# Kernel tuning notes

Hardware: AMD Instinct MI355X
Metric: run time of the kernel (lower is better)

Reference implementation:

```python
import jax, jax.numpy as jnp
import numpy as np

N_NODES = 100000
N_EDGES = 1600000
NUM_FEATURES = 128
HIDDEN = 64
NUM_CLASSES = 16


def setup_inputs() -> dict:
    key = jax.random.key(0)
    k1, k2, k3, k4 = jax.random.split(key, 4)
    x = jax.random.normal(k1, (N_NODES, NUM_FEATURES), dtype=jnp.float32)
    edge_index = jax.random.randint(k2, (2, N_EDGES), 0, N_NODES, dtype=jnp.int64)
    # Glorot-ish scaled weights ([in, out] layout; PyG stores [out,in] but math is x @ W)
    W1 = jax.random.normal(k3, (NUM_FEATURES, HIDDEN), dtype=jnp.float32) * (1.0 / np.sqrt(NUM_FEATURES))
    W2 = jax.random.normal(k4, (HIDDEN, NUM_CLASSES), dtype=jnp.float32) * (1.0 / np.sqrt(HIDDEN))
    return {"x": x, "edge_index": edge_index, "W1": W1, "W2": W2}


def _gcn_conv(x, edge_index, W):
    # GCNConv(add_self_loops=False, bias=False): linear then sym-normalized scatter-add.
    n = x.shape[0]
    row, col = edge_index[0], edge_index[1]  # source -> target
    h = x @ W  # [N, out]
    # degree from unit edge weights scattered on target nodes
    deg = jax.ops.segment_sum(jnp.ones(row.shape[0], dtype=h.dtype), col, num_segments=n)
    deg_inv_sqrt = jnp.where(deg > 0, jax.lax.rsqrt(jnp.maximum(deg, 1.0)), 0.0)
    norm = deg_inv_sqrt[row] * deg_inv_sqrt[col]  # [E]
    msg = h[row] * norm[:, None]  # gather + scale, [E, out]
    return jax.ops.segment_sum(msg, col, num_segments=n)  # scatter-add to targets


def reference(x, edge_index, W1, W2):
    h = _gcn_conv(x, edge_index, W1)
    h = _gcn_conv(h, edge_index, W2)
    return jax.nn.log_softmax(h, axis=1)
```

## Files before the change

kernel.cpp:

```cpp
#include <hip/hip_runtime.h>
#include <hip/hip_bf16.h>
#include <hip/hip_fp16.h>


#define STRIDE 48
#define BCAP   3072
#define SRTCAP 6272


__global__ __launch_bounds__(1024) void k_bucket(const int* __restrict__ ei,
                                                 const void* __restrict__ xv,
                                                 const void* __restrict__ W1v,
                                                 const void* __restrict__ W2v,
                                                 int* __restrict__ flags,
                                                 float* __restrict__ W12,
                                                 int* __restrict__ bcnt,
                                                 int* __restrict__ buf,
                                                 int e, int n, int nb, int epb) {
    __shared__ int hist[1024];
    __shared__ int scn[1024];
    __shared__ int cur[1024];
    __shared__ int gb[1024];
    __shared__ float wtmp[2048];
    __shared__ int srt[SRTCAP];
    __shared__ unsigned short key[SRTCAP];
    __shared__ int sraw, sbad, tot;
    int t = threadIdx.x;
    int b = blockIdx.x;

    if (t == 0) { sraw = 0; sbad = 0; }
    hist[t] = 0;
    __syncthreads();

    long long base_e = (long long)b * epb;
    int myE = e - (int)base_e;
    if (myE > epb) myE = epb;

    if (t < myE) {
        long long i = base_e + t;
        if (ei[2 * (size_t)i + 1] != 0) atomicOr(&sraw, 1);
    }
    if (b < 8) {
        const unsigned short* xs = (const unsigned short*)xv;
        if (t < 1024) {
            unsigned ex2 = (xs[t] >> 7) & 0xFF;
            if (ex2 >= 0x90) atomicOr(&sbad, 1);
        }
    }
    __syncthreads();
    int raw = sraw ? 0 : 1;

    if (b < 8) {
        bool f32 = sbad != 0;
        if (f32) {
            const float* W1 = (const float*)W1v;
            const float* W2 = (const float*)W2v;
            wtmp[t] = W1[b * 1024 + t];
            wtmp[1024 + t] = W2[t];
        } else {
            const __hip_bfloat16* W1 = (const __hip_bfloat16*)W1v;
            const __hip_bfloat16* W2 = (const __hip_bfloat16*)W2v;
            wtmp[t] = __bfloat162float(W1[b * 1024 + t]);
            wtmp[1024 + t] = __bfloat162float(W2[t]);
        }
    }

    int bk[7], rec[7];
#pragma unroll
    for (int j = 0; j < 7; ++j) {
        int li = j * 1024 + t;
        bk[j] = -1;
        if (li < myE) {
            long long i = base_e + li;
            int r, c;
            if (raw) {
                r = ((const int2*)ei)[(size_t)i].x;
                c = ((const int2*)ei)[(size_t)e + i].x;
            } else {
                r = ei[i];
                c = ei[(size_t)e + i];
            }
            if ((unsigned)c < (unsigned)n && (unsigned)r < (unsigned)n) {
                bk[j] = c >> 7;
                rec[j] = ((c & 127) << 17) | r;
                atomicAdd(&hist[bk[j]], 1);
            }
        }
    }
    __syncthreads();

    scn[t] = hist[t];
    __syncthreads();
#pragma unroll
    for (int off = 1; off < 1024; off <<= 1) {
        int add = (t >= off) ? scn[t - off] : 0;
        __syncthreads();
        scn[t] += add;
        __syncthreads();
    }
    {
        int h = hist[t];
        cur[t] = scn[t] - h;
        gb[t] = h ? atomicAdd(&bcnt[t], h) : 0;
        if (t == 1023) tot = scn[1023];
    }
    __syncthreads();

#pragma unroll
    for (int j = 0; j < 7; ++j) {
        if (bk[j] >= 0) {
            int s = atomicAdd(&cur[bk[j]], 1);
            srt[s] = rec[j];
            key[s] = (unsigned short)bk[j];
        }
    }
    __syncthreads();

    int total = tot;
    for (int i = t; i < total; i += 1024) {
        int k = key[i];
        int excl = cur[k] - hist[k];
        int slot = gb[k] + (i - excl);
        if (slot < BCAP) buf[(size_t)k * BCAP + slot] = srt[i];
    }

    if (b < 8 && t < 256) {
        int kl = t >> 4, c = t & 15;
        float acc = 0.0f;
#pragma unroll 8
        for (int f = 0; f < 64; ++f) acc += wtmp[kl * 64 + f] * wtmp[1024 + f * 16 + c];
        W12[(16 * b + kl) * 16 + c] = acc;
        if (b == 0 && t == 0) { flags[0] = sbad; flags[1] = raw; }
    }
}


__global__ __launch_bounds__(256) void k_csr_z(const int* __restrict__ bcnt,
                                               const int* __restrict__ buf,
                                               const void* __restrict__ xv,
                                               const float* __restrict__ W12,
                                               const int* __restrict__ flags,
                                               int* __restrict__ cnt,
                                               int* __restrict__ csr,
                                               __half* __restrict__ z, int n) {
    __shared__ int lcnt[128];
    __shared__ int lcsr[128 * STRIDE];
    __shared__ float ws[2048];
    int t = threadIdx.x;
    int b = blockIdx.x;
    if (t < 128) lcnt[t] = 0;
    int4 zero4 = {0, 0, 0, 0};
    for (int i = t; i < 128 * STRIDE / 4; i += 256) ((int4*)lcsr)[i] = zero4;
    for (int i = t; i < 2048; i += 256) ws[i] = W12[i];
    __syncthreads();

    int m = bcnt[b];
    if (m > BCAP) m = BCAP;
    for (int i = t; i < m; i += 256) {
        int rec = buf[(size_t)b * BCAP + i];
        int cl = rec >> 17;
        int r = rec & 0x1FFFF;
        int slot = atomicAdd(&lcnt[cl], 1);
        if (slot < STRIDE) lcsr[cl * STRIDE + slot] = r;
    }
    __syncthreads();

    {
        int node = (b << 7) + t;
        if (t < 128 && node < n) cnt[node] = lcnt[t];
    }
    const int4* src = (const int4*)lcsr;
    int4* dst = (int4*)csr + (size_t)b * (128 * STRIDE / 4);
    for (int i = t; i < 128 * STRIDE / 4; i += 256) dst[i] = src[i];

    int node_l = t >> 1;
    int kh = t & 1;
    int node0 = (b << 7) + node_l;
    if (node0 >= n) return;
    int node = node0;

    float acc[16];
#pragma unroll
    for (int c = 0; c < 16; ++c) acc[c] = 0.0f;

    if (flags[0]) {
        const float4* x4 = (const float4*)xv + (size_t)node * 32 + kh * 16;
#pragma unroll
        for (int j = 0; j < 16; ++j) {
            float4 v = x4[j];
            float xk[4] = {v.x, v.y, v.z, v.w};
#pragma unroll
            for (int q = 0; q < 4; ++q) {
                const float* w = &ws[(kh * 64 + j * 4 + q) * 16];
                float xx = xk[q];
#pragma unroll
                for (int c = 0; c < 16; ++c) acc[c] += xx * w[c];
            }
        }
    } else {
        const uint4* x4 = (const uint4*)xv + (size_t)node * 16 + kh * 8;
#pragma unroll
        for (int j = 0; j < 8; ++j) {
            uint4 v = x4[j];
            float xk[8];
            xk[0] = __uint_as_float(v.x << 16);
            xk[1] = __uint_as_float(v.x & 0xffff0000u);
            xk[2] = __uint_as_float(v.y << 16);
            xk[3] = __uint_as_float(v.y & 0xffff0000u);
            xk[4] = __uint_as_float(v.z << 16);
            xk[5] = __uint_as_float(v.z & 0xffff0000u);
            xk[6] = __uint_as_float(v.w << 16);
            xk[7] = __uint_as_float(v.w & 0xffff0000u);
#pragma unroll
            for (int q = 0; q < 8; ++q) {
                const float* w = &ws[(kh * 64 + j * 8 + q) * 16];
                float xx = xk[q];
#pragma unroll
                for (int c = 0; c < 16; ++c) acc[c] += xx * w[c];
            }
        }
    }

#pragma unroll
    for (int c = 0; c < 16; ++c) acc[c] += __shfl_xor(acc[c], 1);

    int deg = lcnt[node_l];
    float di = (deg > 0) ? rsqrtf((float)deg) : 0.0f;
    int c0 = kh * 8;
    __half2 hh[4];
#pragma unroll
    for (int j = 0; j < 4; ++j)
        hh[j] = __halves2half2(__float2half(acc[c0 + 2 * j] * di),
                               __float2half(acc[c0 + 2 * j + 1] * di));
    uint4 u;
    u.x = *(unsigned*)&hh[0]; u.y = *(unsigned*)&hh[1];
    u.z = *(unsigned*)&hh[2]; u.w = *(unsigned*)&hh[3];
    ((uint4*)(z + (size_t)node * 16))[kh] = u;
}


__global__ __launch_bounds__(256) void k_agg1b(const int* __restrict__ cnt,
                                               const int* __restrict__ csr,
                                               const __half* __restrict__ z,
                                               __half* __restrict__ z2, int n) {
    int t = threadIdx.x;
    int wid = t >> 6, lane = t & 63;
    int half = lane >> 5, l5 = lane & 31;
    int node0 = blockIdx.x * 8 + wid * 2 + half;
    int node = node0 < n ? node0 : n - 1;
    int id  = csr[(size_t)node * STRIDE + l5];
    int id2 = csr[(size_t)node * STRIDE + 32 + (l5 & 15)];
    int deg = cnt[node];
    float di = (deg > 0) ? rsqrtf((float)deg) : 0.0f;
    int m = deg < STRIDE ? deg : STRIDE;
    int sub = l5 >> 3, f2 = l5 & 7;
    int base = half << 5;
    const __half2* zp = (const __half2*)z;
    float ax = 0.0f, ay = 0.0f;
#pragma unroll
    for (int j = 0; j < 24; j += 4) {
        int s = __shfl(id, base + j + sub);
        float2 v = __half22float2(zp[(size_t)s * 8 + f2]);
        bool ok = (j + sub) < m;
        ax += ok ? v.x : 0.0f;
        ay += ok ? v.y : 0.0f;
    }
    for (int j = 24; j < m; j += 4) {
        int sidx = j + sub;
        int s = (j < 32) ? __shfl(id, base + sidx)
                         : __shfl(id2, base + (sidx & 15));
        if (sidx < m) {
            float2 v = __half22float2(zp[(size_t)s * 8 + f2]);
            ax += v.x;
            ay += v.y;
        }
    }
    ax += __shfl_xor(ax, 8);  ay += __shfl_xor(ay, 8);
    ax += __shfl_xor(ax, 16); ay += __shfl_xor(ay, 16);
    float s2 = di * di;
    if (node0 < n && l5 < 8)
        ((__half2*)z2)[(size_t)node * 8 + l5] =
            __halves2half2(__float2half(ax * s2), __float2half(ay * s2));
}


__global__ __launch_bounds__(256) void k_agg2b(const int* __restrict__ cnt,
                                               const int* __restrict__ csr,
                                               const __half* __restrict__ z2,
                                               const int* __restrict__ flags,
                                               void* __restrict__ outv, int n) {
    int t = threadIdx.x;
    int wid = t >> 6, lane = t & 63;
    int half = lane >> 5, l5 = lane & 31;
    int node0 = blockIdx.x * 8 + wid * 2 + half;
    int node = node0 < n ? node0 : n - 1;
    int id  = csr[(size_t)node * STRIDE + l5];
    int id2 = csr[(size_t)node * STRIDE + 32 + (l5 & 15)];
    int deg = cnt[node];
    float di = (deg > 0) ? rsqrtf((float)deg) : 0.0f;
    int m = deg < STRIDE ? deg : STRIDE;
    int sub = l5 >> 3, f2 = l5 & 7;
    int base = half << 5;
    const __half2* zp = (const __half2*)z2;
    float ax = 0.0f, ay = 0.0f;
#pragma unroll
    for (int j = 0; j < 24; j += 4) {
        int s = __shfl(id, base + j + sub);
        float2 v = __half22float2(zp[(size_t)s * 8 + f2]);
        bool ok = (j + sub) < m;
        ax += ok ? v.x : 0.0f;
        ay += ok ? v.y : 0.0f;
    }
    for (int j = 24; j < m; j += 4) {
        int sidx = j + sub;
        int s = (j < 32) ? __shfl(id, base + sidx)
                         : __shfl(id2, base + (sidx & 15));
        if (sidx < m) {
            float2 v = __half22float2(zp[(size_t)s * 8 + f2]);
            ax += v.x;
            ay += v.y;
        }
    }
    ax += __shfl_xor(ax, 8);  ay += __shfl_xor(ay, 8);
    ax += __shfl_xor(ax, 16); ay += __shfl_xor(ay, 16);
    float vx = ax * di, vy = ay * di;
    float mx = fmaxf(vx, vy);
#pragma unroll
    for (int d = 1; d <= 4; d <<= 1) mx = fmaxf(mx, __shfl_xor(mx, d));
    float es = __expf(vx - mx) + __expf(vy - mx);
#pragma unroll
    for (int d = 1; d <= 4; d <<= 1) es += __shfl_xor(es, d);
    float ls = __logf(es);
    float rx = vx - mx - ls, ry = vy - mx - ls;
    if (node0 < n && l5 < 8) {
        if (flags[0]) {
            float2 r; r.x = rx; r.y = ry;
            ((float2*)outv)[(size_t)node * 8 + l5] = r;
        } else {
            __hip_bfloat162 hh;
            hh.x = __float2bfloat16(rx);
            hh.y = __float2bfloat16(ry);
            ((__hip_bfloat162*)outv)[(size_t)node * 8 + l5] = hh;
        }
    }
}


extern "C" void kernel_launch(void* const* d_in, const int* in_sizes, int n_in,
                              void* d_out, int out_size, void* d_ws, size_t ws_size,
                              hipStream_t stream) {
    const int F = 128, C = 16;
    int n = in_sizes[0] / F;
    int e = in_sizes[1] / 2;
    int nb = (n + 127) >> 7;

    const void* x = d_in[0];
    const int* ei = (const int*)d_in[1];
    const void* W1 = d_in[2];
    const void* W2 = d_in[3];

    char* p = (char*)d_ws;
    auto carve = [&](size_t bytes) {
        char* r = p;
        p += (bytes + 255) & ~(size_t)255;
        return r;
    };
    int*    flags = (int*)  carve(256);
    int*    bcnt  = (int*)  carve((size_t)nb * 4);
    int*    cnt   = (int*)  carve((size_t)n * 4);
    float*  W12   = (float*)carve(128 * 16 * 4);
    int*    csr   = (int*)  carve(((size_t)nb * 128 * STRIDE + 64) * 4);
    __half* z     = (__half*)carve((size_t)n * C * 2);
    size_t buf_sz = (size_t)nb * BCAP * 4;
    size_t z2_sz = (size_t)n * C * 2;
    char* regionB = carve(buf_sz > z2_sz ? buf_sz : z2_sz);
    int*    buf = (int*)regionB;
    __half* z2  = (__half*)regionB;
    (void)ws_size;

    int gb_bucket = (e + SRTCAP - 1) / SRTCAP;
    if (gb_bucket < 256) gb_bucket = 256;
    int epb = (e + gb_bucket - 1) / gb_bucket;

    hipMemsetAsync(bcnt, 0, (size_t)nb * 4, stream);
    k_bucket<<<gb_bucket, 1024, 0, stream>>>(ei, x, W1, W2, flags, W12, bcnt, buf, e, n, nb, epb);
    k_csr_z<<<nb, 256, 0, stream>>>(bcnt, buf, x, W12, flags, cnt, csr, z, n);
    k_agg1b<<<(n + 7) / 8, 256, 0, stream>>>(cnt, csr, z, z2, n);
    k_agg2b<<<(n + 7) / 8, 256, 0, stream>>>(cnt, csr, z2, flags, d_out, n);
}
```

Before: 159.8 us.

## Rebuild per-bucket CSR in shared memory inside each aggregation kernel

The first kernel no longer writes a global padded CSR and count array. It now only counts degrees. Each aggregation kernel instead rebuilds its bucket's adjacency lists in LDS from the bucket buffer and then processes 128 nodes per 512-thread block. This removes the global CSR write and the two strided CSR reads, and buf and z2 get separate workspace. In exchange the bucket-to-CSR scatter is done twice, each block uses a large LDS footprint, and the block count drops, which may cost occupancy and latency hiding.

```diff
diff --git a/kernel.cpp b/kernel.cpp
--- a/kernel.cpp
+++ b/kernel.cpp
@@ -42,10 +42,8 @@
     }
     if (b < 8) {
         const unsigned short* xs = (const unsigned short*)xv;
-        if (t < 1024) {
-            unsigned ex2 = (xs[t] >> 7) & 0xFF;
-            if (ex2 >= 0x90) atomicOr(&sbad, 1);
-        }
+        unsigned ex2 = (xs[t] >> 7) & 0xFF;
+        if (ex2 >= 0x90) atomicOr(&sbad, 1);
     }
     __syncthreads();
     int raw = sraw ? 0 : 1;
@@ -135,22 +133,17 @@
 }
 
 
-__global__ __launch_bounds__(256) void k_csr_z(const int* __restrict__ bcnt,
-                                               const int* __restrict__ buf,
-                                               const void* __restrict__ xv,
-                                               const float* __restrict__ W12,
-                                               const int* __restrict__ flags,
-                                               int* __restrict__ cnt,
-                                               int* __restrict__ csr,
-                                               __half* __restrict__ z, int n) {
+__global__ __launch_bounds__(256) void k_zd(const int* __restrict__ bcnt,
+                                            const int* __restrict__ buf,
+                                            const void* __restrict__ xv,
+                                            const float* __restrict__ W12,
+                                            const int* __restrict__ flags,
+                                            __half* __restrict__ z, int n) {
     __shared__ int lcnt[128];
-    __shared__ int lcsr[128 * STRIDE];
     __shared__ float ws[2048];
     int t = threadIdx.x;
     int b = blockIdx.x;
     if (t < 128) lcnt[t] = 0;
-    int4 zero4 = {0, 0, 0, 0};
-    for (int i = t; i < 128 * STRIDE / 4; i += 256) ((int4*)lcsr)[i] = zero4;
     for (int i = t; i < 2048; i += 256) ws[i] = W12[i];
     __syncthreads();
 
@@ -158,20 +151,9 @@
     if (m > BCAP) m = BCAP;
     for (int i = t; i < m; i += 256) {
         int rec = buf[(size_t)b * BCAP + i];
-        int cl = rec >> 17;
-        int r = rec & 0x1FFFF;
-        int slot = atomicAdd(&lcnt[cl], 1);
-        if (slot < STRIDE) lcsr[cl * STRIDE + slot] = r;
-    }
-    __syncthreads();
-
-    {
-        int node = (b << 7) + t;
-        if (t < 128 && node < n) cnt[node] = lcnt[t];
-    }
-    const int4* src = (const int4*)lcsr;
-    int4* dst = (int4*)csr + (size_t)b * (128 * STRIDE / 4);
-    for (int i = t; i < 128 * STRIDE / 4; i += 256) dst[i] = src[i];
+        atomicAdd(&lcnt[rec >> 17], 1);
+    }
+    __syncthreads();
 
     int node_l = t >> 1;
     int kh = t & 1;
@@ -239,108 +221,147 @@
 }
 
 
-__global__ __launch_bounds__(256) void k_agg1b(const int* __restrict__ cnt,
-                                               const int* __restrict__ csr,
+__global__ __launch_bounds__(512) void k_agg1n(const int* __restrict__ bcnt,
+                                               const int* __restrict__ buf,
                                                const __half* __restrict__ z,
                                                __half* __restrict__ z2, int n) {
+    __shared__ int lcnt[128];
+    __shared__ int lcsr[128 * STRIDE];
     int t = threadIdx.x;
+    int b = blockIdx.x;
+    if (t < 128) lcnt[t] = 0;
+    int4 zero4 = {0, 0, 0, 0};
+    for (int i = t; i < 128 * STRIDE / 4; i += 512) ((int4*)lcsr)[i] = zero4;
+    __syncthreads();
+
+    int m = bcnt[b];
+    if (m > BCAP) m = BCAP;
+    for (int i = t; i < m; i += 512) {
+        int rec = buf[(size_t)b * BCAP + i];
+        int cl = rec >> 17;
+        int r = rec & 0x1FFFF;
+        int slot = atomicAdd(&lcnt[cl], 1);
+        if (slot < STRIDE) lcsr[cl * STRIDE + slot] = r;
+    }
+    __syncthreads();
+
     int wid = t >> 6, lane = t & 63;
     int half = lane >> 5, l5 = lane & 31;
-    int node0 = blockIdx.x * 8 + wid * 2 + half;
-    int node = node0 < n ? node0 : n - 1;
-    int id  = csr[(size_t)node * STRIDE + l5];
-    int id2 = csr[(size_t)node * STRIDE + 32 + (l5 & 15)];
-    int deg = cnt[node];
-    float di = (deg > 0) ? rsqrtf((float)deg) : 0.0f;
-    int m = deg < STRIDE ? deg : STRIDE;
     int sub = l5 >> 3, f2 = l5 & 7;
-    int base = half << 5;
     const __half2* zp = (const __half2*)z;
-    float ax = 0.0f, ay = 0.0f;
-#pragma unroll
-    for (int j = 0; j < 24; j += 4) {
-        int s = __shfl(id, base + j + sub);
-        float2 v = __half22float2(zp[(size_t)s * 8 + f2]);
-        bool ok = (j + sub) < m;
-        ax += ok ? v.x : 0.0f;
-        ay += ok ? v.y : 0.0f;
-    }
-    for (int j = 24; j < m; j += 4) {
-        int sidx = j + sub;
-        int s = (j < 32) ? __shfl(id, base + sidx)
-                         : __shfl(id2, base + (sidx & 15));
-        if (sidx < m) {
+#pragma unroll
+    for (int it = 0; it < 8; ++it) {
+        int node_l = it * 16 + wid * 2 + half;
+        int node0 = (b << 7) + node_l;
+        int deg = lcnt[node_l];
+        float di = (deg > 0) ? rsqrtf((float)deg) : 0.0f;
+        int mm = deg < STRIDE ? deg : STRIDE;
+        int lb = node_l * STRIDE;
+        float ax = 0.0f, ay = 0.0f;
+#pragma unroll
+        for (int j = 0; j < 24; j += 4) {
+            int s = lcsr[lb + j + sub];
             float2 v = __half22float2(zp[(size_t)s * 8 + f2]);
-            ax += v.x;
-            ay += v.y;
-        }
-    }
-    ax += __shfl_xor(ax, 8);  ay += __shfl_xor(ay, 8);
-    ax += __shfl_xor(ax, 16); ay += __shfl_xor(ay, 16);
-    float s2 = di * di;
-    if (node0 < n && l5 < 8)
-        ((__half2*)z2)[(size_t)node * 8 + l5] =
-            __halves2half2(__float2half(ax * s2), __float2half(ay * s2));
+            bool ok = (j + sub) < mm;
+            ax += ok ? v.x : 0.0f;
+            ay += ok ? v.y : 0.0f;
+        }
+        for (int j = 24; j < mm; j += 4) {
+            int sidx = j + sub;
+            if (sidx < mm) {
+                int s = lcsr[lb + sidx];
+                float2 v = __half22float2(zp[(size_t)s * 8 + f2]);
+                ax += v.x;
+                ay += v.y;
+            }
+        }
+        ax += __shfl_xor(ax, 8);  ay += __shfl_xor(ay, 8);
+        ax += __shfl_xor(ax, 16); ay += __shfl_xor(ay, 16);
+        float s2 = di * di;
+        if (node0 < n && l5 < 8)
+            ((__half2*)z2)[(size_t)node0 * 8 + l5] =
+                __halves2half2(__float2half(ax * s2), __float2half(ay * s2));
+    }
 }
 
 
-__global__ __launch_bounds__(256) void k_agg2b(const int* __restrict__ cnt,
-                                               const int* __restrict__ csr,
+__global__ __launch_bounds__(512) void k_agg2n(const int* __restrict__ bcnt,
+                                               const int* __restrict__ buf,
                                                const __half* __restrict__ z2,
                                                const int* __restrict__ flags,
                                                void* __restrict__ outv, int n) {
+    __shared__ int lcnt[128];
+    __shared__ int lcsr[128 * STRIDE];
     int t = threadIdx.x;
+    int b = blockIdx.x;
+    if (t < 128) lcnt[t] = 0;
+    int4 zero4 = {0, 0, 0, 0};
+    for (int i = t; i < 128 * STRIDE / 4; i += 512) ((int4*)lcsr)[i] = zero4;
+    __syncthreads();
+
+    int m = bcnt[b];
+    if (m > BCAP) m = BCAP;
+    for (int i = t; i < m; i += 512) {
+        int rec = buf[(size_t)b * BCAP + i];
+        int cl = rec >> 17;
+        int r = rec & 0x1FFFF;
+        int slot = atomicAdd(&lcnt[cl], 1);
+        if (slot < STRIDE) lcsr[cl * STRIDE + slot] = r;
+    }
+    __syncthreads();
+
     int wid = t >> 6, lane = t & 63;
     int half = lane >> 5, l5 = lane & 31;
-    int node0 = blockIdx.x * 8 + wid * 2 + half;
-    int node = node0 < n ? node0 : n - 1;
-    int id  = csr[(size_t)node * STRIDE + l5];
-    int id2 = csr[(size_t)node * STRIDE + 32 + (l5 & 15)];
-    int deg = cnt[node];
-    float di = (deg > 0) ? rsqrtf((float)deg) : 0.0f;
-    int m = deg < STRIDE ? deg : STRIDE;
     int sub = l5 >> 3, f2 = l5 & 7;
-    int base = half << 5;
     const __half2* zp = (const __half2*)z2;
-    float ax = 0.0f, ay = 0.0f;
-#pragma unroll
-    for (int j = 0; j < 24; j += 4) {
-        int s = __shfl(id, base + j + sub);
-        float2 v = __half22float2(zp[(size_t)s * 8 + f2]);
-        bool ok = (j + sub) < m;
-        ax += ok ? v.x : 0.0f;
-        ay += ok ? v.y : 0.0f;
-    }
-    for (int j = 24; j < m; j += 4) {
-        int sidx = j + sub;
-        int s = (j < 32) ? __shfl(id, base + sidx)
-                         : __shfl(id2, base + (sidx & 15));
-        if (sidx < m) {
+    bool f32o = flags[0] != 0;
+#pragma unroll
+    for (int it = 0; it < 8; ++it) {
+        int node_l = it * 16 + wid * 2 + half;
+        int node0 = (b << 7) + node_l;
+        int deg = lcnt[node_l];
+        float di = (deg > 0) ? rsqrtf((float)deg) : 0.0f;
+        int mm = deg < STRIDE ? deg : STRIDE;
+        int lb = node_l * STRIDE;
+        float ax = 0.0f, ay = 0.0f;
+#pragma unroll
+        for (int j = 0; j < 24; j += 4) {
+            int s = lcsr[lb + j + sub];
             float2 v = __half22float2(zp[(size_t)s * 8 + f2]);
-            ax += v.x;
-            ay += v.y;
-        }
-    }
-    ax += __shfl_xor(ax, 8);  ay += __shfl_xor(ay, 8);
-    ax += __shfl_xor(ax, 16); ay += __shfl_xor(ay, 16);
-    float vx = ax * di, vy = ay * di;
-    float mx = fmaxf(vx, vy);
-#pragma unroll
-    for (int d = 1; d <= 4; d <<= 1) mx = fmaxf(mx, __shfl_xor(mx, d));
-    float es = __expf(vx - mx) + __expf(vy - mx);
-#pragma unroll
-    for (int d = 1; d <= 4; d <<= 1) es += __shfl_xor(es, d);
-    float ls = __logf(es);
-    float rx = vx - mx - ls, ry = vy - mx - ls;
-    if (node0 < n && l5 < 8) {
-        if (flags[0]) {
-            float2 r; r.x = rx; r.y = ry;
-            ((float2*)outv)[(size_t)node * 8 + l5] = r;
-        } else {
-            __hip_bfloat162 hh;
-            hh.x = __float2bfloat16(rx);
-            hh.y = __float2bfloat16(ry);
-            ((__hip_bfloat162*)outv)[(size_t)node * 8 + l5] = hh;
+            bool ok = (j + sub) < mm;
+            ax += ok ? v.x : 0.0f;
+            ay += ok ? v.y : 0.0f;
+        }
+        for (int j = 24; j < mm; j += 4) {
+            int sidx = j + sub;
+            if (sidx < mm) {
+                int s = lcsr[lb + sidx];
+                float2 v = __half22float2(zp[(size_t)s * 8 + f2]);
+                ax += v.x;
+                ay += v.y;
+            }
+        }
+        ax += __shfl_xor(ax, 8);  ay += __shfl_xor(ay, 8);
+        ax += __shfl_xor(ax, 16); ay += __shfl_xor(ay, 16);
+        float vx = ax * di, vy = ay * di;
+        float mx = fmaxf(vx, vy);
+#pragma unroll
+        for (int d = 1; d <= 4; d <<= 1) mx = fmaxf(mx, __shfl_xor(mx, d));
+        float es = __expf(vx - mx) + __expf(vy - mx);
+#pragma unroll
+        for (int d = 1; d <= 4; d <<= 1) es += __shfl_xor(es, d);
+        float ls = __logf(es);
+        float rx = vx - mx - ls, ry = vy - mx - ls;
+        if (node0 < n && l5 < 8) {
+            if (f32o) {
+                float2 r; r.x = rx; r.y = ry;
+                ((float2*)outv)[(size_t)node0 * 8 + l5] = r;
+            } else {
+                __hip_bfloat162 hh;
+                hh.x = __float2bfloat16(rx);
+                hh.y = __float2bfloat16(ry);
+                ((__hip_bfloat162*)outv)[(size_t)node0 * 8 + l5] = hh;
+            }
         }
     }
 }
@@ -367,15 +388,10 @@
     };
     int*    flags = (int*)  carve(256);
     int*    bcnt  = (int*)  carve((size_t)nb * 4);
-    int*    cnt   = (int*)  carve((size_t)n * 4);
     float*  W12   = (float*)carve(128 * 16 * 4);
-    int*    csr   = (int*)  carve(((size_t)nb * 128 * STRIDE + 64) * 4);
+    int*    buf   = (int*)  carve((size_t)nb * BCAP * 4);
     __half* z     = (__half*)carve((size_t)n * C * 2);
-    size_t buf_sz = (size_t)nb * BCAP * 4;
-    size_t z2_sz = (size_t)n * C * 2;
-    char* regionB = carve(buf_sz > z2_sz ? buf_sz : z2_sz);
-    int*    buf = (int*)regionB;
-    __half* z2  = (__half*)regionB;
+    __half* z2    = (__half*)carve((size_t)n * C * 2);
     (void)ws_size;
 
     int gb_bucket = (e + SRTCAP - 1) / SRTCAP;
@@ -384,7 +400,7 @@
 
     hipMemsetAsync(bcnt, 0, (size_t)nb * 4, stream);
     k_bucket<<<gb_bucket, 1024, 0, stream>>>(ei, x, W1, W2, flags, W12, bcnt, buf, e, n, nb, epb);
-    k_csr_z<<<nb, 256, 0, stream>>>(bcnt, buf, x, W12, flags, cnt, csr, z, n);
-    k_agg1b<<<(n + 7) / 8, 256, 0, stream>>>(cnt, csr, z, z2, n);
-    k_agg2b<<<(n + 7) / 8, 256, 0, stream>>>(cnt, csr, z2, flags, d_out, n);
+    k_zd<<<nb, 256, 0, stream>>>(bcnt, buf, x, W12, flags, z, n);
+    k_agg1n<<<nb, 512, 0, stream>>>(bcnt, buf, z, z2, n);
+    k_agg2n<<<nb, 512, 0, stream>>>(bcnt, buf, z2, flags, d_out, n);
 }
```

Result: slower. 164.0 us (+2.6%).
